# Kernel tuning notes

Hardware: AMD Instinct MI355X
Metric: run time of the kernel (lower is better)

The kernel has to match this reference:

```python
import jax, jax.numpy as jnp
import numpy as np

NUM_EMBEDDINGS = 1024
EMBEDDING_DIM = 64
COMMITMENT_COST = 0.25


def setup_inputs() -> dict:
    key = jax.random.key(0)
    k1, k2 = jax.random.split(key)
    inputs = jax.random.normal(k1, (32, 4096, EMBEDDING_DIM), dtype=jnp.float32)
    embeddings = jax.random.normal(k2, (NUM_EMBEDDINGS, EMBEDDING_DIM), dtype=jnp.float32)
    return {"inputs": inputs, "embeddings": embeddings}


def _l2_normalize(x, axis=-1, eps=1e-12):
    # matches F.normalize(p=2): x / max(||x||, eps)
    n = jnp.sqrt(jnp.sum(x * x, axis=axis, keepdims=True))
    return x / jnp.maximum(n, eps)


def reference(inputs, embeddings):
    input_shape = inputs.shape
    flat = inputs.reshape(-1, EMBEDDING_DIM)            # [N, D]
    flat_n = _l2_normalize(flat, axis=1)                # [N, D]
    emb_n = _l2_normalize(embeddings, axis=1)           # [K, D]

    # squared euclidean distances between normalized vectors: [N, K]
    d = (jnp.sum(flat_n * flat_n, axis=1, keepdims=True)
         + jnp.sum(emb_n * emb_n, axis=1)
         - 2.0 * flat_n @ emb_n.T)
    idx = jnp.argmin(d, axis=1)                         # [N] int

    quantized = embeddings[idx]                         # [N, D] gather

    e_latent_loss = jnp.mean((jax.lax.stop_gradient(quantized) - flat) ** 2)
    # straight-through estimator
    quantized_ste = flat + jax.lax.stop_gradient(quantized - flat)
    q_latent_loss = jnp.mean((quantized_ste - jax.lax.stop_gradient(flat)) ** 2)
    vq_loss = q_latent_loss + COMMITMENT_COST * e_latent_loss

    quantized_out = quantized_ste.reshape(input_shape)

    counts = jnp.bincount(idx, length=NUM_EMBEDDINGS).astype(jnp.float32)
    avg_probs = counts / idx.shape[0]
    perplexity = jnp.exp(-jnp.sum(avg_probs * jnp.log(avg_probs + 1e-10)))
    codebook_usage = jnp.sum(avg_probs > 0).astype(jnp.float32) / NUM_EMBEDDINGS

    return quantized_out, idx, vq_loss, perplexity, codebook_usage
```

## Files before the change

### kernel.cpp

```cpp
#include <hip/hip_runtime.h>
#include <hip/hip_bf16.h>

#define NQ       131072
#define KC       1024
#define DIM      64
#define MARGIN_P 1.5e-4f
#define RGRID    2048

typedef __attribute__((ext_vector_type(8))) short  s8bf;
typedef __attribute__((ext_vector_type(4))) float  f32x4;

union BF8 { s8bf v; unsigned short u[8]; };

__device__ __forceinline__ unsigned short f2bf_u(float f) {
    union { __hip_bfloat16 h; unsigned short u; } cv;
    cv.h = __float2bfloat16(f);
    return cv.u;
}
__device__ __forceinline__ float bfu2f(unsigned short u) {
    union { __hip_bfloat16 h; unsigned short u; } cv;
    cv.u = u;
    return __bfloat162float(cv.h);
}
__device__ __forceinline__ void gl_lds16(const float4* g, float4* l) {
    __builtin_amdgcn_global_load_lds(
        (const __attribute__((address_space(1))) unsigned int*)g,
        (__attribute__((address_space(3))) unsigned int*)l, 16, 0, 0);
}

__global__ __launch_bounds__(256) void k_prep(const float* __restrict__ emb,
                                              unsigned short* __restrict__ wB,
                                              double* __restrict__ eT,
                                              double* __restrict__ wB2D,
                                              int* __restrict__ counts,
                                              int* __restrict__ nflag,
                                              float* __restrict__ lossp) {
    const int tid = threadIdx.x;
    if (blockIdx.x == 0) {
        #pragma unroll
        for (int i = 0; i < 4; ++i) counts[tid * 4 + i] = 0;
        if (tid == 0) { *nflag = 0; *lossp = 0.f; }
    }
    int c = blockIdx.x * 256 + tid;
    if (c >= KC) return;
    float e[DIM];
    const float4* ep = reinterpret_cast<const float4*>(emb + (size_t)c * DIM);
    #pragma unroll
    for (int i = 0; i < 16; ++i) {
        float4 t = ep[i];
        e[4*i+0] = t.x; e[4*i+1] = t.y; e[4*i+2] = t.z; e[4*i+3] = t.w;
    }
    float s = 0.f;
    #pragma unroll
    for (int i = 0; i < DIM; ++i) s += e[i] * e[i];
    float inv = 1.0f / fmaxf(sqrtf(s), 1e-12f);
    const int t = c >> 4, col = c & 15;
    #pragma unroll
    for (int k = 0; k < DIM; ++k) {
        float h = e[k] * inv;
        unsigned short hi = f2bf_u(h);
        unsigned short lo = f2bf_u(h - bfu2f(hi));
        int s_ = k >> 5, g = (k >> 3) & 3, j = k & 7;
        int ln = col + 16 * g;
        wB[((t*4 + s_*2 + 0) * 64 + ln) * 8 + j] = hi;
        wB[((t*4 + s_*2 + 1) * 64 + ln) * 8 + j] = lo;
    }
    double sd = 0.0;
    #pragma unroll
    for (int i = 0; i < DIM; ++i) sd += (double)e[i] * (double)e[i];
    double dnd = fmax(sqrt(sd), 1e-12);
    double b2 = 0.0;
    #pragma unroll
    for (int i = 0; i < DIM; ++i) {
        double eh = (double)e[i] / dnd;
        eT[(size_t)i * KC + c] = eh;
        b2 += eh * eh;
    }
    wB2D[c] = b2;
}

__global__ __launch_bounds__(256) void k_assign(const float* __restrict__ inp,
                                                const unsigned short* __restrict__ wB,
                                                float* __restrict__ idx_out,
                                                int* __restrict__ flag_list,
                                                int* __restrict__ nflag) {
    __shared__ s8bf Bt[2048];
    const int tid  = threadIdx.x;
    const int lane = tid & 63, wv = tid >> 6;
    const int col  = lane & 15, g  = lane >> 4;
    const int qbase = blockIdx.x * 128 + wv * 32;

    BF8 ah[2][2], al[2][2];
    #pragma unroll
    for (int s = 0; s < 2; ++s) {
        const float4* q4 = reinterpret_cast<const float4*>(inp + (size_t)(qbase + 16*s + col) * DIM);
        float4 xa = q4[2*g], xb = q4[2*g + 1], ya = q4[8 + 2*g], yb = q4[9 + 2*g];
        float x[16] = { xa.x, xa.y, xa.z, xa.w, xb.x, xb.y, xb.z, xb.w,
                        ya.x, ya.y, ya.z, ya.w, yb.x, yb.y, yb.z, yb.w };
        float sq = 0.f;
        #pragma unroll
        for (int i = 0; i < 16; ++i) sq += x[i] * x[i];
        sq += __shfl_xor(sq, 16);
        sq += __shfl_xor(sq, 32);
        float inv = 1.0f / fmaxf(sqrtf(sq), 1e-12f);
        #pragma unroll
        for (int i = 0; i < 8; ++i) {
            float h0 = x[i] * inv, h1 = x[8 + i] * inv;
            unsigned short hi0 = f2bf_u(h0);
            unsigned short hi1 = f2bf_u(h1);
            ah[s][0].u[i] = hi0;  al[s][0].u[i] = f2bf_u(h0 - bfu2f(hi0));
            ah[s][1].u[i] = hi1;  al[s][1].u[i] = f2bf_u(h1 - bfu2f(hi1));
        }
    }

    int best[2][4], best2[2][4];
    #pragma unroll
    for (int s = 0; s < 2; ++s)
        #pragma unroll
        for (int r = 0; r < 4; ++r) { best[s][r] = 0x7FFFFFFF; best2[s][r] = 0x7FFFFFFF; }

    for (int ch = 0; ch < 8; ++ch) {
        __syncthreads();
        const float4* src = reinterpret_cast<const float4*>(wB) + (size_t)ch * 2048;
        float4* dst = reinterpret_cast<float4*>(Bt);
        #pragma unroll
        for (int i = 0; i < 8; ++i) {
            int idx = i * 256 + tid;
            gl_lds16(&src[idx], &dst[idx]);
        }
        __syncthreads();

        for (int nt = 0; nt < 8; ++nt) {
            s8bf bh0 = Bt[(nt*4 + 0) * 64 + lane];
            s8bf bl0 = Bt[(nt*4 + 1) * 64 + lane];
            s8bf bh1 = Bt[(nt*4 + 2) * 64 + lane];
            s8bf bl1 = Bt[(nt*4 + 3) * 64 + lane];
            const int gt = ch * 8 + nt;
            #pragma unroll
            for (int s = 0; s < 2; ++s) {
                f32x4 acc = {0.f, 0.f, 0.f, 0.f};
                acc = __builtin_amdgcn_mfma_f32_16x16x32_bf16(ah[s][0].v, bh0, acc, 0, 0, 0);
                acc = __builtin_amdgcn_mfma_f32_16x16x32_bf16(ah[s][1].v, bh1, acc, 0, 0, 0);
                acc = __builtin_amdgcn_mfma_f32_16x16x32_bf16(ah[s][0].v, bl0, acc, 0, 0, 0);
                acc = __builtin_amdgcn_mfma_f32_16x16x32_bf16(ah[s][1].v, bl1, acc, 0, 0, 0);
                acc = __builtin_amdgcn_mfma_f32_16x16x32_bf16(al[s][0].v, bh0, acc, 0, 0, 0);
                acc = __builtin_amdgcn_mfma_f32_16x16x32_bf16(al[s][1].v, bh1, acc, 0, 0, 0);
                #pragma unroll
                for (int r = 0; r < 4; ++r) {
                    float dp = fmaf(-2.0f, acc[r], 3.0f);
                    int p = (__float_as_int(dp) & 0xFFFFFFC0) | gt;
                    int mn = min(best[s][r], p);
                    int mx = max(best[s][r], p);
                    best[s][r]  = mn;
                    best2[s][r] = min(best2[s][r], mx);
                }
            }
        }
    }

    int colb[2][4];
    #pragma unroll
    for (int s = 0; s < 2; ++s)
        #pragma unroll
        for (int r = 0; r < 4; ++r) colb[s][r] = col;

    #pragma unroll
    for (int s = 0; s < 2; ++s) {
        #pragma unroll
        for (int off = 1; off < 16; off <<= 1) {
            #pragma unroll
            for (int r = 0; r < 4; ++r) {
                int ob  = __shfl_xor(best[s][r],  off);
                int ob2 = __shfl_xor(best2[s][r], off);
                int oc  = __shfl_xor(colb[s][r],  off);
                int bo  = best[s][r];
                colb[s][r]  = (ob < bo) ? oc : colb[s][r];
                best[s][r]  = min(bo, ob);
                best2[s][r] = min(min(best2[s][r], ob2), max(bo, ob));
            }
        }
        #pragma unroll
        for (int r = 0; r < 4; ++r) {
            if (col == r) {
                int   q  = qbase + 16*s + 4*g + r;
                int   pk = best[s][r];
                float d1 = __int_as_float(pk & 0xFFFFFFC0);
                float d2 = __int_as_float(best2[s][r] & 0xFFFFFFC0);
                int code = ((pk & 63) << 4) | colb[s][r];
                idx_out[q] = (float)code;
                if (d2 - d1 < MARGIN_P || d1 >= 4.0f) {
                    int slot = atomicAdd(nflag, 1);
                    flag_list[slot] = q;
                }
            }
        }
    }
}

__global__ __launch_bounds__(256) void k_rescue(const float* __restrict__ inp,
                                                const double* __restrict__ eT,
                                                const double* __restrict__ wB2D,
                                                const int* __restrict__ flag_list,
                                                const int* __restrict__ nflag,
                                                float* __restrict__ idx_out) {
    __shared__ double xh[DIM];
    __shared__ double Ash;
    __shared__ double sdw[4];
    __shared__ int    siw[4];
    const int tid = threadIdx.x;
    const int lane = tid & 63, wv = tid >> 6;
    const int n = *nflag;

    for (int j = blockIdx.x; j < n; j += gridDim.x) {
        const int q = flag_list[j];
        if (tid < 64) {
            double xv = (double)inp[(size_t)q * DIM + tid];
            double s = xv * xv;
            #pragma unroll
            for (int off = 32; off; off >>= 1) s += __shfl_xor(s, off);
            double dn = fmax(sqrt(s), 1e-12);
            double h  = xv / dn;
            xh[tid] = h;
            double a = h * h;
            #pragma unroll
            for (int off = 32; off; off >>= 1) a += __shfl_xor(a, off);
            if (tid == 0) Ash = a;
        }
        __syncthreads();
        const double A = Ash;

        double dot0 = 0.0, dot1 = 0.0, dot2 = 0.0, dot3 = 0.0;
        #pragma unroll 8
        for (int i = 0; i < DIM; ++i) {
            double xi = xh[i];
            const double* row = eT + (size_t)i * KC + tid;
            dot0 += xi * row[0];
            dot1 += xi * row[256];
            dot2 += xi * row[512];
            dot3 += xi * row[768];
        }
        double bd = 1e300; int bi = 1 << 30;
        double d0 = (A + wB2D[tid      ]) - 2.0 * dot0;
        double d1 = (A + wB2D[tid + 256]) - 2.0 * dot1;
        double d2 = (A + wB2D[tid + 512]) - 2.0 * dot2;
        double d3 = (A + wB2D[tid + 768]) - 2.0 * dot3;
        if (d0 < bd) { bd = d0; bi = tid;       }
        if (d1 < bd) { bd = d1; bi = tid + 256; }
        if (d2 < bd) { bd = d2; bi = tid + 512; }
        if (d3 < bd) { bd = d3; bi = tid + 768; }
        #pragma unroll
        for (int off = 1; off < 64; off <<= 1) {
            double od = __shfl_xor(bd, off);
            int    oi = __shfl_xor(bi, off);
            if (od < bd || (od == bd && oi < bi)) { bd = od; bi = oi; }
        }
        if (lane == 0) { sdw[wv] = bd; siw[wv] = bi; }
        __syncthreads();
        if (tid == 0) {
            double B = sdw[0]; int I = siw[0];
            #pragma unroll
            for (int i = 1; i < 4; ++i)
                if (sdw[i] < B || (sdw[i] == B && siw[i] < I)) { B = sdw[i]; I = siw[i]; }
            idx_out[q] = (float)I;
        }
        __syncthreads();
    }
}

__global__ __launch_bounds__(256) void k_gather_loss(const float* __restrict__ inp,
                                                     const float* __restrict__ emb,
                                                     const float* __restrict__ idx_out,
                                                     float* __restrict__ qout,
                                                     float* __restrict__ loss) {
    const int gid = blockIdx.x * 256 + threadIdx.x;
    float lsum = 0.f;
    for (int e4 = gid; e4 < NQ * 16; e4 += 524288) {
        int   qi = e4 >> 4;
        int   d4 = e4 & 15;
        int   k  = ((int)idx_out[qi]) & (KC - 1);
        float4 qv = reinterpret_cast<const float4*>(emb + (size_t)k * DIM)[d4];
        float4 fv = reinterpret_cast<const float4*>(inp)[e4];
        float ux = qv.x - fv.x, uy = qv.y - fv.y, uz = qv.z - fv.z, uw = qv.w - fv.w;
        lsum += ux*ux + uy*uy + uz*uz + uw*uw;
        reinterpret_cast<float4*>(qout)[e4] = qv;
    }
    #pragma unroll
    for (int off = 32; off; off >>= 1) lsum += __shfl_xor(lsum, off);
    __shared__ float wsum[4];
    int wid = threadIdx.x >> 6, lane = threadIdx.x & 63;
    if (lane == 0) wsum[wid] = lsum;
    __syncthreads();
    if (threadIdx.x == 0)
        atomicAdd(loss, (wsum[0] + wsum[1]) + (wsum[2] + wsum[3]));
}

__global__ __launch_bounds__(256) void k_hist(const float* __restrict__ idx_out,
                                              int* __restrict__ counts) {
    __shared__ int h[KC];
    const int tid = threadIdx.x;
    for (int i = tid; i < KC; i += 256) h[i] = 0;
    __syncthreads();
    const int qb = blockIdx.x * 2048;
    for (int i = tid; i < 2048; i += 256)
        atomicAdd(&h[((int)idx_out[qb + i]) & (KC - 1)], 1);
    __syncthreads();
    for (int i = tid; i < KC; i += 256) {
        int v = h[i];
        if (v) atomicAdd(&counts[i], v);
    }
}

__global__ __launch_bounds__(1024) void k_stats2(const int* __restrict__ counts,
                                                 float* __restrict__ out3) {
    int t = threadIdx.x;
    int c = counts[t];
    float p    = (float)c * (1.0f / (float)NQ);
    float ent  = p * logf(p + 1e-10f);
    float used = (c > 0) ? 1.0f : 0.0f;
    #pragma unroll
    for (int off = 32; off; off >>= 1) {
        ent  += __shfl_xor(ent, off);
        used += __shfl_xor(used, off);
    }
    __shared__ float se[16], su[16];
    int w = t >> 6, l = t & 63;
    if (l == 0) { se[w] = ent; su[w] = used; }
    __syncthreads();
    if (t == 0) {
        float E = 0.f, U = 0.f;
        #pragma unroll
        for (int i = 0; i < 16; ++i) { E += se[i]; U += su[i]; }
        float L = out3[0];
        out3[0] = L * 1.25f / 8388608.0f;
        out3[1] = expf(-E);
        out3[2] = U * (1.0f / 1024.0f);
    }
}

extern "C" void kernel_launch(void* const* d_in, const int* in_sizes, int n_in,
                              void* d_out, int out_size, void* d_ws, size_t ws_size,
                              hipStream_t stream) {
    const float* inp = (const float*)d_in[0];
    const float* emb = (const float*)d_in[1];

    float*  qout      = (float*)d_out;
    int*    flag_list = (int*)d_out;
    double* eT        = (double*)((float*)d_out + 1048576);
    float*  idx_out   = (float*)d_out + 8388608;
    float*  out3      = (float*)d_out + 8519680;

    int*            counts = (int*)d_ws;
    unsigned short* wB     = (unsigned short*)((char*)d_ws + 4096);
    double*         wB2D   = (double*)((char*)d_ws + 266240);
    int*            nflag  = (int*)((char*)d_ws + 274432);

    hipLaunchKernelGGL(k_prep,        dim3(4),     dim3(256),  0, stream,
                       emb, wB, eT, wB2D, counts, nflag, out3);
    hipLaunchKernelGGL(k_assign,      dim3(1024),  dim3(256),  0, stream,
                       inp, wB, idx_out, flag_list, nflag);
    hipLaunchKernelGGL(k_rescue,      dim3(RGRID), dim3(256),  0, stream,
                       inp, eT, wB2D, flag_list, nflag, idx_out);
    hipLaunchKernelGGL(k_gather_loss, dim3(2048),  dim3(256),  0, stream,
                       inp, emb, idx_out, qout, out3);
    hipLaunchKernelGGL(k_hist,        dim3(64),    dim3(256),  0, stream, idx_out, counts);
    hipLaunchKernelGGL(k_stats2,      dim3(1),     dim3(1024), 0, stream, counts, out3);
}
```

Baseline: 126.7 us.

## Double-buffer codebook chunks in LDS and fuse histogram into gather kernel

```diff
diff --git a/kernel.cpp b/kernel.cpp
--- a/kernel.cpp
+++ b/kernel.cpp
@@ -84,7 +84,7 @@
                                                 float* __restrict__ idx_out,
                                                 int* __restrict__ flag_list,
                                                 int* __restrict__ nflag) {
-    __shared__ s8bf Bt[2048];
+    __shared__ s8bf Bt[2][2048];
     const int tid  = threadIdx.x;
     const int lane = tid & 63, wv = tid >> 6;
     const int col  = lane & 15, g  = lane >> 4;
@@ -119,22 +119,33 @@
         #pragma unroll
         for (int r = 0; r < 4; ++r) { best[s][r] = 0x7FFFFFFF; best2[s][r] = 0x7FFFFFFF; }
 
+    const float4* wB4 = reinterpret_cast<const float4*>(wB);
+
+    #pragma unroll
+    for (int i = 0; i < 8; ++i) {
+        int idx = i * 256 + tid;
+        gl_lds16(wB4 + idx, reinterpret_cast<float4*>(&Bt[0][0]) + idx);
+    }
+    asm volatile("s_waitcnt vmcnt(0)" ::: "memory");
+    __builtin_amdgcn_s_barrier();
+    asm volatile("" ::: "memory");
+
+    int cur = 0;
     for (int ch = 0; ch < 8; ++ch) {
-        __syncthreads();
-        const float4* src = reinterpret_cast<const float4*>(wB) + (size_t)ch * 2048;
-        float4* dst = reinterpret_cast<float4*>(Bt);
-        #pragma unroll
-        for (int i = 0; i < 8; ++i) {
-            int idx = i * 256 + tid;
-            gl_lds16(&src[idx], &dst[idx]);
-        }
-        __syncthreads();
-
+        if (ch < 7) {
+            const float4* src = wB4 + (size_t)(ch + 1) * 2048;
+            float4* dst = reinterpret_cast<float4*>(&Bt[cur ^ 1][0]);
+            #pragma unroll
+            for (int i = 0; i < 8; ++i) {
+                int idx = i * 256 + tid;
+                gl_lds16(src + idx, dst + idx);
+            }
+        }
         for (int nt = 0; nt < 8; ++nt) {
-            s8bf bh0 = Bt[(nt*4 + 0) * 64 + lane];
-            s8bf bl0 = Bt[(nt*4 + 1) * 64 + lane];
-            s8bf bh1 = Bt[(nt*4 + 2) * 64 + lane];
-            s8bf bl1 = Bt[(nt*4 + 3) * 64 + lane];
+            s8bf bh0 = Bt[cur][(nt*4 + 0) * 64 + lane];
+            s8bf bl0 = Bt[cur][(nt*4 + 1) * 64 + lane];
+            s8bf bh1 = Bt[cur][(nt*4 + 2) * 64 + lane];
+            s8bf bl1 = Bt[cur][(nt*4 + 3) * 64 + lane];
             const int gt = ch * 8 + nt;
             #pragma unroll
             for (int s = 0; s < 2; ++s) {
@@ -156,6 +167,12 @@
                 }
             }
         }
+        if (ch < 7) {
+            asm volatile("s_waitcnt vmcnt(0)" ::: "memory");
+            __builtin_amdgcn_s_barrier();
+            asm volatile("" ::: "memory");
+            cur ^= 1;
+        }
     }
 
     int colb[2][4];
@@ -271,8 +288,14 @@
                                                      const float* __restrict__ emb,
                                                      const float* __restrict__ idx_out,
                                                      float* __restrict__ qout,
-                                                     float* __restrict__ loss) {
-    const int gid = blockIdx.x * 256 + threadIdx.x;
+                                                     float* __restrict__ loss,
+                                                     int* __restrict__ counts) {
+    __shared__ int h[KC];
+    const int tid = threadIdx.x;
+    for (int i = tid; i < KC; i += 256) h[i] = 0;
+    __syncthreads();
+
+    const int gid = blockIdx.x * 256 + tid;
     float lsum = 0.f;
     for (int e4 = gid; e4 < NQ * 16; e4 += 524288) {
         int   qi = e4 >> 4;
@@ -283,31 +306,21 @@
         float ux = qv.x - fv.x, uy = qv.y - fv.y, uz = qv.z - fv.z, uw = qv.w - fv.w;
         lsum += ux*ux + uy*uy + uz*uz + uw*uw;
         reinterpret_cast<float4*>(qout)[e4] = qv;
-    }
-    #pragma unroll
-    for (int off = 32; off; off >>= 1) lsum += __shfl_xor(lsum, off);
-    __shared__ float wsum[4];
-    int wid = threadIdx.x >> 6, lane = threadIdx.x & 63;
-    if (lane == 0) wsum[wid] = lsum;
-    __syncthreads();
-    if (threadIdx.x == 0)
-        atomicAdd(loss, (wsum[0] + wsum[1]) + (wsum[2] + wsum[3]));
-}
-
-__global__ __launch_bounds__(256) void k_hist(const float* __restrict__ idx_out,
-                                              int* __restrict__ counts) {
-    __shared__ int h[KC];
-    const int tid = threadIdx.x;
-    for (int i = tid; i < KC; i += 256) h[i] = 0;
-    __syncthreads();
-    const int qb = blockIdx.x * 2048;
-    for (int i = tid; i < 2048; i += 256)
-        atomicAdd(&h[((int)idx_out[qb + i]) & (KC - 1)], 1);
+        if (d4 == 0) atomicAdd(&h[k], 1);
+    }
     __syncthreads();
     for (int i = tid; i < KC; i += 256) {
         int v = h[i];
         if (v) atomicAdd(&counts[i], v);
     }
+    #pragma unroll
+    for (int off = 32; off; off >>= 1) lsum += __shfl_xor(lsum, off);
+    __shared__ float wsum[4];
+    int wid = tid >> 6, lane = tid & 63;
+    if (lane == 0) wsum[wid] = lsum;
+    __syncthreads();
+    if (tid == 0)
+        atomicAdd(loss, (wsum[0] + wsum[1]) + (wsum[2] + wsum[3]));
 }
 
 __global__ __launch_bounds__(1024) void k_stats2(const int* __restrict__ counts,
@@ -361,7 +374,6 @@
     hipLaunchKernelGGL(k_rescue,      dim3(RGRID), dim3(256),  0, stream,
                        inp, eT, wB2D, flag_list, nflag, idx_out);
     hipLaunchKernelGGL(k_gather_loss, dim3(2048),  dim3(256),  0, stream,
-                       inp, emb, idx_out, qout, out3);
-    hipLaunchKernelGGL(k_hist,        dim3(64),    dim3(256),  0, stream, idx_out, counts);
+                       inp, emb, idx_out, qout, out3, counts);
     hipLaunchKernelGGL(k_stats2,      dim3(1),     dim3(1024), 0, stream, counts, out3);
 }
```

Result: no change. 124.7 us (-1.5%).

## Fold distance affine into MFMA init, use med3 for top-2, fuse histogram into gather

Applied to the files above, without the earlier changes.

```diff
diff --git a/kernel.cpp b/kernel.cpp
--- a/kernel.cpp
+++ b/kernel.cpp
@@ -4,7 +4,7 @@
 #define NQ       131072
 #define KC       1024
 #define DIM      64
-#define MARGIN_P 1.5e-4f
+#define MARGIN_A 7.5e-5f
 #define RGRID    2048
 
 typedef __attribute__((ext_vector_type(8))) short  s8bf;
@@ -102,10 +102,10 @@
         for (int i = 0; i < 16; ++i) sq += x[i] * x[i];
         sq += __shfl_xor(sq, 16);
         sq += __shfl_xor(sq, 32);
-        float inv = 1.0f / fmaxf(sqrtf(sq), 1e-12f);
+        float ninv = -1.0f / fmaxf(sqrtf(sq), 1e-12f);
         #pragma unroll
         for (int i = 0; i < 8; ++i) {
-            float h0 = x[i] * inv, h1 = x[8 + i] * inv;
+            float h0 = x[i] * ninv, h1 = x[8 + i] * ninv;
             unsigned short hi0 = f2bf_u(h0);
             unsigned short hi1 = f2bf_u(h1);
             ah[s][0].u[i] = hi0;  al[s][0].u[i] = f2bf_u(h0 - bfu2f(hi0));
@@ -126,7 +126,7 @@
         #pragma unroll
         for (int i = 0; i < 8; ++i) {
             int idx = i * 256 + tid;
-            gl_lds16(&src[idx], &dst[idx]);
+            gl_lds16(src + idx, dst + idx);
         }
         __syncthreads();
 
@@ -138,7 +138,7 @@
             const int gt = ch * 8 + nt;
             #pragma unroll
             for (int s = 0; s < 2; ++s) {
-                f32x4 acc = {0.f, 0.f, 0.f, 0.f};
+                f32x4 acc = {1.5f, 1.5f, 1.5f, 1.5f};
                 acc = __builtin_amdgcn_mfma_f32_16x16x32_bf16(ah[s][0].v, bh0, acc, 0, 0, 0);
                 acc = __builtin_amdgcn_mfma_f32_16x16x32_bf16(ah[s][1].v, bh1, acc, 0, 0, 0);
                 acc = __builtin_amdgcn_mfma_f32_16x16x32_bf16(ah[s][0].v, bl0, acc, 0, 0, 0);
@@ -147,12 +147,13 @@
                 acc = __builtin_amdgcn_mfma_f32_16x16x32_bf16(al[s][1].v, bh1, acc, 0, 0, 0);
                 #pragma unroll
                 for (int r = 0; r < 4; ++r) {
-                    float dp = fmaf(-2.0f, acc[r], 3.0f);
-                    int p = (__float_as_int(dp) & 0xFFFFFFC0) | gt;
-                    int mn = min(best[s][r], p);
-                    int mx = max(best[s][r], p);
-                    best[s][r]  = mn;
-                    best2[s][r] = min(best2[s][r], mx);
+                    int p = (__float_as_int(acc[r]) & 0xFFFFFFC0) | gt;
+                    int bo = best[s][r];
+                    int b2n;
+                    asm("v_med3_i32 %0, %1, %2, %3"
+                        : "=v"(b2n) : "v"(bo), "v"(best2[s][r]), "v"(p));
+                    best2[s][r] = b2n;
+                    best[s][r]  = min(bo, p);
                 }
             }
         }
@@ -184,11 +185,11 @@
             if (col == r) {
                 int   q  = qbase + 16*s + 4*g + r;
                 int   pk = best[s][r];
-                float d1 = __int_as_float(pk & 0xFFFFFFC0);
-                float d2 = __int_as_float(best2[s][r] & 0xFFFFFFC0);
+                float a1 = __int_as_float(pk & 0xFFFFFFC0);
+                float a2 = __int_as_float(best2[s][r] & 0xFFFFFFC0);
                 int code = ((pk & 63) << 4) | colb[s][r];
                 idx_out[q] = (float)code;
-                if (d2 - d1 < MARGIN_P || d1 >= 4.0f) {
+                if (a2 - a1 < MARGIN_A) {
                     int slot = atomicAdd(nflag, 1);
                     flag_list[slot] = q;
                 }
@@ -271,8 +272,14 @@
                                                      const float* __restrict__ emb,
                                                      const float* __restrict__ idx_out,
                                                      float* __restrict__ qout,
-                                                     float* __restrict__ loss) {
-    const int gid = blockIdx.x * 256 + threadIdx.x;
+                                                     float* __restrict__ loss,
+                                                     int* __restrict__ counts) {
+    __shared__ int h[KC];
+    const int tid = threadIdx.x;
+    for (int i = tid; i < KC; i += 256) h[i] = 0;
+    __syncthreads();
+
+    const int gid = blockIdx.x * 256 + tid;
     float lsum = 0.f;
     for (int e4 = gid; e4 < NQ * 16; e4 += 524288) {
         int   qi = e4 >> 4;
@@ -283,31 +290,21 @@
         float ux = qv.x - fv.x, uy = qv.y - fv.y, uz = qv.z - fv.z, uw = qv.w - fv.w;
         lsum += ux*ux + uy*uy + uz*uz + uw*uw;
         reinterpret_cast<float4*>(qout)[e4] = qv;
-    }
-    #pragma unroll
-    for (int off = 32; off; off >>= 1) lsum += __shfl_xor(lsum, off);
-    __shared__ float wsum[4];
-    int wid = threadIdx.x >> 6, lane = threadIdx.x & 63;
-    if (lane == 0) wsum[wid] = lsum;
-    __syncthreads();
-    if (threadIdx.x == 0)
-        atomicAdd(loss, (wsum[0] + wsum[1]) + (wsum[2] + wsum[3]));
-}
-
-__global__ __launch_bounds__(256) void k_hist(const float* __restrict__ idx_out,
-                                              int* __restrict__ counts) {
-    __shared__ int h[KC];
-    const int tid = threadIdx.x;
-    for (int i = tid; i < KC; i += 256) h[i] = 0;
-    __syncthreads();
-    const int qb = blockIdx.x * 2048;
-    for (int i = tid; i < 2048; i += 256)
-        atomicAdd(&h[((int)idx_out[qb + i]) & (KC - 1)], 1);
+        if (d4 == 0) atomicAdd(&h[k], 1);
+    }
     __syncthreads();
     for (int i = tid; i < KC; i += 256) {
         int v = h[i];
         if (v) atomicAdd(&counts[i], v);
     }
+    #pragma unroll
+    for (int off = 32; off; off >>= 1) lsum += __shfl_xor(lsum, off);
+    __shared__ float wsum[4];
+    int wid = tid >> 6, lane = tid & 63;
+    if (lane == 0) wsum[wid] = lsum;
+    __syncthreads();
+    if (tid == 0)
+        atomicAdd(loss, (wsum[0] + wsum[1]) + (wsum[2] + wsum[3]));
 }
 
 __global__ __launch_bounds__(1024) void k_stats2(const int* __restrict__ counts,
@@ -361,7 +358,6 @@
     hipLaunchKernelGGL(k_rescue,      dim3(RGRID), dim3(256),  0, stream,
                        inp, eT, wB2D, flag_list, nflag, idx_out);
     hipLaunchKernelGGL(k_gather_loss, dim3(2048),  dim3(256),  0, stream,
-                       inp, emb, idx_out, qout, out3);
-    hipLaunchKernelGGL(k_hist,        dim3(64),    dim3(256),  0, stream, idx_out, counts);
+                       inp, emb, idx_out, qout, out3, counts);
     hipLaunchKernelGGL(k_stats2,      dim3(1),     dim3(1024), 0, stream, counts, out3);
 }
```

After: 127.2 us. About the same (+0.4%).
